# Optimization experiments

Measured on AMD Instinct MI355X. Metric: run time of the kernel, lower is better.

The kernel has to match this reference:

```python
import jax, jax.numpy as jnp
import numpy as np

V = 32000  # vocab_size
H = 5      # hidden_size (hardcoded-tiny per original module)
T = 1024   # encoder input length
L = 1024   # decoder output length


def setup_inputs() -> dict:
    key = jax.random.key(0)
    ks = jax.random.split(key, 11)
    f32 = jnp.float32
    return {
        "x": jax.random.normal(ks[0], (T, V), f32),
        "l": L,
        "Eg_en": jax.random.normal(ks[1], (H, V), f32),
        "Eg_de": jax.random.normal(ks[2], (V, H), f32),
        "cg_de": jax.random.normal(ks[3], (V,), f32),
        "Wg_en": jax.random.normal(ks[4], (3, H, H), f32),
        "Ug_en": jax.random.normal(ks[5], (3, H, H), f32),
        "bg_en": jax.random.normal(ks[6], (3, H), f32),
        "Wg_de": jax.random.normal(ks[7], (3, H, H), f32),
        "Ug_de": jax.random.normal(ks[8], (3, H, H), f32),
        "bg_de": jax.random.normal(ks[9], (3, H), f32),
    }


def reference(x, l, Eg_en, Eg_de, cg_de, Wg_en, Ug_en, bg_en, Wg_de, Ug_de, bg_de):
    sig = jax.nn.sigmoid
    h = Eg_en.shape[0]

    # ---- encoder: GRU-style recurrence over x rows ----
    # fold all V->h projections into one big matmul (same math as per-step matvec)
    xe_all = x @ Eg_en.T  # [T, h]

    def enc_step(s, xe):
        z = sig(Wg_en[0] @ xe + Ug_en[0] @ s + bg_en[0])
        r = sig(Wg_en[1] @ xe + Ug_en[1] @ s + bg_en[1])
        c = jnp.tanh(Wg_en[2] @ xe + Ug_en[2] @ (s * r) + bg_en[2])
        return z * s + (1.0 - z) * c, None

    s_last, _ = jax.lax.scan(enc_step, jnp.zeros((h,), x.dtype), xe_all)

    # first decoded word
    w1 = jax.nn.relu(Eg_de @ s_last + cg_de)  # [V]

    # ---- decoder: feeds its own output back as next input ----
    def dec_step(carry, _):
        w_prev, s = carry
        xe = Eg_en @ w_prev  # [h]
        z = sig(Wg_de[0] @ xe + Ug_de[0] @ s + bg_de[0])
        r = sig(Wg_de[1] @ xe + Ug_de[1] @ s + bg_de[1])
        c = jnp.tanh(Wg_de[2] @ xe + Ug_de[2] @ (s * r) + bg_de[2])
        s_new = z * s + (1.0 - z) * c
        w = jax.nn.relu(Eg_de @ s_new + cg_de)
        return (w, s_new), w

    (_, _), words = jax.lax.scan(dec_step, (w1, s_last), None, length=l)  # [l, V]

    # original returns cat(w1, words[:-1])
    return jnp.concatenate([w1[None, :], words[:-1]], axis=0)  # [l, V]
```

## Files before the change

kernel.cpp:

```cpp
#include <hip/hip_runtime.h>

#define VSZ 32000
#define TT 1024
#define LL 1024
#define NCH 64
#define CHL 16
#define TROW 4

typedef float f32x4 __attribute__((ext_vector_type(4)));

__device__ __forceinline__ float fast_sigmoid(float x){
  return __builtin_amdgcn_rcpf(1.0f + __expf(-x));
}
__device__ __forceinline__ float fast_tanh(float x){
  float e = __expf(2.0f*x);
  return 1.0f - 2.0f*__builtin_amdgcn_rcpf(e + 1.0f);
}

__device__ __forceinline__ float rl(float v, int l){
  return __uint_as_float((unsigned)__builtin_amdgcn_readlane((int)__float_as_uint(v), l));
}

__device__ __forceinline__ void load_gru_w(const float* __restrict__ W,
                                           const float* __restrict__ U,
                                           const float* __restrict__ b,
                                           int lane, float Wr[5], float U1r[5], float U2r[5], float& bb)
{
  int g = lane / 5;
  int i = lane - g*5;
  bool okl = (lane < 15);
  int base = okl ? (g*25 + i*5) : 0;
  int bidx = okl ? (g*5 + i) : 0;
  #pragma unroll
  for (int j=0;j<5;j++){
    float w  = W[base + j];
    float u  = U[base + j];
    float u2 = U[50 + i*5 + j];
    Wr[j]  = okl ? w : 0.0f;
    U1r[j] = (okl && g < 2) ? u  : 0.0f;
    U2r[j] = (okl && g == 2) ? u2 : 0.0f;
  }
  bb = okl ? b[bidx] : 0.0f;
}

__device__ __forceinline__ void gru_step_exact(const float xe[5], float s[5], bool& conv,
                                               const float Wr[5], const float U1r[5],
                                               const float U2r[5], float bb)
{
  float acc = bb;
  #pragma unroll
  for (int j=0;j<5;j++) acc += Wr[j]*xe[j];
  #pragma unroll
  for (int j=0;j<5;j++) acc += U1r[j]*s[j];
  float zr = fast_sigmoid(acc);
  float rr[5];
  #pragma unroll
  for (int j=0;j<5;j++) rr[j] = rl(zr, 5+j);
  float acc2 = acc;
  #pragma unroll
  for (int j=0;j<5;j++) acc2 += U2r[j]*(s[j]*rr[j]);
  float cv = fast_tanh(acc2);
  conv = true;
  #pragma unroll
  for (int j=0;j<5;j++){
    float zj = rl(zr, j);
    float cj = rl(cv, 10+j);
    float ns = zj*s[j] + (1.0f - zj)*cj;
    conv = conv && (__float_as_uint(ns) == __float_as_uint(s[j]));
    s[j] = ns;
  }
}

__device__ __forceinline__ void enc_step(float pre, float s[5],
                                         const float U1r[5], const float U2r[5])
{
  float a0 = U1r[0]*s[0] + U1r[1]*s[1];
  float a1 = U1r[2]*s[2] + U1r[3]*s[3];
  float acc = pre + a0 + a1 + U1r[4]*s[4];
  float zr = fast_sigmoid(acc);
  float rr[5];
  #pragma unroll
  for (int j=0;j<5;j++) rr[j] = rl(zr, 5+j);
  float acc2 = acc;
  #pragma unroll
  for (int j=0;j<5;j++) acc2 += U2r[j]*(s[j]*rr[j]);
  float cv = fast_tanh(acc2);
  #pragma unroll
  for (int j=0;j<5;j++){
    float zj = rl(zr, j);
    float cj = rl(cv, 10+j);
    s[j] = zj*s[j] + (1.0f - zj)*cj;
  }
}

__global__ __launch_bounds__(256) void matmul_pre(const float* __restrict__ x,
                                                  const float* __restrict__ Eg_en,
                                                  const float* __restrict__ W,
                                                  const float* __restrict__ b,
                                                  float* __restrict__ pre_all,
                                                  float* __restrict__ eslots_f)
{
  const int t0 = blockIdx.x * TROW;
  const int tid = threadIdx.x;
  const int lane = tid & 63, wave = tid >> 6;
  if (blockIdx.x == 0){
    #pragma unroll
    for (int k=0;k<4;k++) eslots_f[k*256 + tid] = 0.0f;
  }
  float acc[TROW][5];
  #pragma unroll
  for (int r=0;r<TROW;r++)
    #pragma unroll
    for (int h=0;h<5;h++) acc[r][h] = 0.0f;

  #pragma unroll 2
  for (int j = tid; j < VSZ/4; j += 256){
    f32x4 ev[5];
    #pragma unroll
    for (int h=0;h<5;h++) ev[h] = ((const f32x4*)(Eg_en + (size_t)h*VSZ))[j];
    #pragma unroll
    for (int r=0;r<TROW;r++){
      f32x4 xv = ((const f32x4*)(x + (size_t)(t0+r)*VSZ))[j];
      #pragma unroll
      for (int h=0;h<5;h++)
        acc[r][h] += xv.x*ev[h].x + xv.y*ev[h].y + xv.z*ev[h].z + xv.w*ev[h].w;
    }
  }
  #pragma unroll
  for (int m=1;m<64;m<<=1){
    #pragma unroll
    for (int r=0;r<TROW;r++)
      #pragma unroll
      for (int h=0;h<5;h++) acc[r][h] += __shfl_xor(acc[r][h], m, 64);
  }
  __shared__ float part[4][TROW][5];
  __shared__ float xe_s[TROW][5];
  if (lane == 0){
    #pragma unroll
    for (int r=0;r<TROW;r++)
      #pragma unroll
      for (int h=0;h<5;h++) part[wave][r][h] = acc[r][h];
  }
  __syncthreads();
  if (tid < TROW*5){
    int r = tid/5, h = tid - r*5;
    xe_s[r][h] = part[0][r][h] + part[1][r][h] + part[2][r][h] + part[3][r][h];
  }
  __syncthreads();
  if (tid < TROW*16){
    int r = tid >> 4, k = tid & 15;
    if (k < 15){
      int g = k/5, i = k - g*5;
      float p = b[g*5+i];
      #pragma unroll
      for (int j=0;j<5;j++) p += W[g*25 + i*5 + j] * xe_s[r][j];
      pre_all[(t0+r)*16 + k] = p;
    }
  }
}

__global__ void enc_kernel(const float* __restrict__ pre_all,
                           float* __restrict__ s_enc,
                           float* __restrict__ dslots_f,
                           unsigned long long* __restrict__ eslots,
                           const float* __restrict__ U)
{
  const int w = blockIdx.x;
  const int lane = threadIdx.x;
  { int idx = w*64 + lane; if (idx < 2048) dslots_f[idx] = 0.0f; }

  int g = lane/5, i = lane - g*5;
  bool okl = (lane < 15);
  float U1r[5], U2r[5];
  #pragma unroll
  for (int j=0;j<5;j++){
    int base = okl ? (g*25 + i*5) : 0;
    float u  = U[base + j];
    float u2 = U[50 + i*5 + j];
    U1r[j] = (okl && g < 2) ? u  : 0.0f;
    U2r[j] = (okl && g == 2) ? u2 : 0.0f;
  }

  float prc[CHL];
  #pragma unroll
  for (int k=0;k<CHL;k++) prc[k] = okl ? pre_all[(w*CHL + k)*16 + lane] : 0.0f;

  float s_in[5] = {0,0,0,0,0};
  float prev[5] = {0,0,0,0,0};
  unsigned p = 0;
  for(;;){
    p++;
    float s[5];
    #pragma unroll
    for (int j=0;j<5;j++) s[j] = s_in[j];
    #pragma unroll
    for (int k=0;k<CHL;k++) enc_step(prc[k], s, U1r, U2r);

    bool stable = (p > 1);
    #pragma unroll
    for (int j=0;j<5;j++)
      stable = stable && (__float_as_uint(s[j]) == __float_as_uint(prev[j]));
    #pragma unroll
    for (int j=0;j<5;j++) prev[j] = s[j];

    const unsigned long long hi = ((unsigned long long)((p<<1) | (stable?1u:0u))) << 32;
    if (lane == 0){
      unsigned long long* wp = eslots + (size_t)w*8;
      #pragma unroll
      for (int j=0;j<5;j++)
        __hip_atomic_store(wp+j, hi | (unsigned long long)__float_as_uint(s[j]),
                           __ATOMIC_RELAXED, __HIP_MEMORY_SCOPE_AGENT);
    }

    const unsigned long long* rp = eslots + (size_t)lane*8;
    unsigned long long w0,w1,w2,w3,w4;
    for(;;){
      w0 = __hip_atomic_load(rp+0, __ATOMIC_RELAXED, __HIP_MEMORY_SCOPE_AGENT);
      w1 = __hip_atomic_load(rp+1, __ATOMIC_RELAXED, __HIP_MEMORY_SCOPE_AGENT);
      w2 = __hip_atomic_load(rp+2, __ATOMIC_RELAXED, __HIP_MEMORY_SCOPE_AGENT);
      w3 = __hip_atomic_load(rp+3, __ATOMIC_RELAXED, __HIP_MEMORY_SCOPE_AGENT);
      w4 = __hip_atomic_load(rp+4, __ATOMIC_RELAXED, __HIP_MEMORY_SCOPE_AGENT);
      bool ok = ((unsigned)(w0>>33)==p) & ((unsigned)(w1>>33)==p) & ((unsigned)(w2>>33)==p)
              & ((unsigned)(w3>>33)==p) & ((unsigned)(w4>>33)==p);
      if (__all(ok)) break;
    }
    bool slot_stable = ((w0>>32)&1ull) != 0;
    bool gstable = __all(slot_stable);

    float xin[5];
    xin[0] = __uint_as_float((unsigned)w0);
    xin[1] = __uint_as_float((unsigned)w1);
    xin[2] = __uint_as_float((unsigned)w2);
    xin[3] = __uint_as_float((unsigned)w3);
    xin[4] = __uint_as_float((unsigned)w4);

    if (gstable){
      if (w == 0 && lane == 0){
        #pragma unroll
        for (int j=0;j<5;j++) s_enc[j] = rl(xin[j], 63);
      }
      break;
    }
    if (w > 0){
      #pragma unroll
      for (int j=0;j<5;j++) s_in[j] = rl(xin[j], w-1);
    }
  }
}

__global__ __launch_bounds__(256, 1) void dec_kernel(
    const float* __restrict__ Eg_en, const float* __restrict__ Eg_de,
    const float* __restrict__ cg_de,
    const float* __restrict__ W, const float* __restrict__ U, const float* __restrict__ b,
    const float* __restrict__ s_enc,
    unsigned long long* __restrict__ slots,
    float* __restrict__ out,
    int* __restrict__ t_conv_out)
{
  const int wg = blockIdx.x;
  const int tid = threadIdx.x;
  const int lane = tid & 63;
  const int wave = tid >> 6;
  const int slot_id = wg*4 + wave;

  float Wr[5], U1r[5], U2r[5], bb;
  load_gru_w(W, U, b, lane, Wr, U1r, U2r, bb);

  const bool act = (tid < 250);
  const int v0 = wg*2000 + tid*8;
  float de[8][5], en[5][8], cb[8];
  if (act){
    #pragma unroll
    for (int k=0;k<8;k++){
      #pragma unroll
      for (int j=0;j<5;j++) de[k][j] = Eg_de[(v0+k)*5 + j];
      cb[k] = cg_de[v0+k];
    }
    #pragma unroll
    for (int h=0;h<5;h++){
      #pragma unroll
      for (int k=0;k<8;k++) en[h][k] = Eg_en[h*VSZ + v0 + k];
    }
  } else {
    #pragma unroll
    for (int k=0;k<8;k++){
      cb[k] = 0.0f;
      #pragma unroll
      for (int j=0;j<5;j++) de[k][j] = 0.0f;
    }
    #pragma unroll
    for (int h=0;h<5;h++){
      #pragma unroll
      for (int k=0;k<8;k++) en[h][k] = 0.0f;
    }
  }

  float s[5];
  #pragma unroll
  for (int j=0;j<5;j++) s[j] = s_enc[j];

  for (int t=0; t<LL; t++){
    float px[5] = {0,0,0,0,0};
    float o[8];
    #pragma unroll
    for (int k=0;k<8;k++){
      float u = cb[k];
      #pragma unroll
      for (int j=0;j<5;j++) u += de[k][j]*s[j];
      u = fmaxf(u, 0.0f);
      o[k] = u;
      #pragma unroll
      for (int h=0;h<5;h++) px[h] += u*en[h][k];
    }
    if (act){
      f32x4* po = (f32x4*)(out + (size_t)t*VSZ + v0);
      f32x4 oa = {o[0], o[1], o[2], o[3]};
      f32x4 ob = {o[4], o[5], o[6], o[7]};
      po[0] = oa; po[1] = ob;
    }
    if (t == LL-1){
      if (wg == 0 && tid == 0) *t_conv_out = LL-1;
      break;
    }

    #pragma unroll
    for (int m=1;m<64;m<<=1){
      #pragma unroll
      for (int h=0;h<5;h++) px[h] += __shfl_xor(px[h], m, 64);
    }

    const unsigned long long tg = (unsigned long long)(t+1);
    if (lane == 0){
      unsigned long long* wp = slots + ((size_t)(t&1)*64 + slot_id)*8;
      #pragma unroll
      for (int j=0;j<5;j++)
        __hip_atomic_store(wp+j, (tg<<32) | (unsigned long long)__float_as_uint(px[j]),
                           __ATOMIC_RELAXED, __HIP_MEMORY_SCOPE_AGENT);
    }

    const unsigned long long* rp = slots + ((size_t)(t&1)*64 + lane)*8;
    unsigned long long w0,w1,w2,w3,w4;
    for(;;){
      w0 = __hip_atomic_load(rp+0, __ATOMIC_RELAXED, __HIP_MEMORY_SCOPE_AGENT);
      w1 = __hip_atomic_load(rp+1, __ATOMIC_RELAXED, __HIP_MEMORY_SCOPE_AGENT);
      w2 = __hip_atomic_load(rp+2, __ATOMIC_RELAXED, __HIP_MEMORY_SCOPE_AGENT);
      w3 = __hip_atomic_load(rp+3, __ATOMIC_RELAXED, __HIP_MEMORY_SCOPE_AGENT);
      w4 = __hip_atomic_load(rp+4, __ATOMIC_RELAXED, __HIP_MEMORY_SCOPE_AGENT);
      bool ok = ((w0>>32)==tg) & ((w1>>32)==tg) & ((w2>>32)==tg)
              & ((w3>>32)==tg) & ((w4>>32)==tg);
      if (__all(ok)) break;
    }
    float xe[5];
    xe[0] = __uint_as_float((unsigned)w0);
    xe[1] = __uint_as_float((unsigned)w1);
    xe[2] = __uint_as_float((unsigned)w2);
    xe[3] = __uint_as_float((unsigned)w3);
    xe[4] = __uint_as_float((unsigned)w4);
    #pragma unroll
    for (int m=1;m<64;m<<=1){
      #pragma unroll
      for (int j=0;j<5;j++) xe[j] += __shfl_xor(xe[j], m, 64);
    }

    bool conv;
    gru_step_exact(xe, s, conv, Wr, U1r, U2r, bb);

    if (conv){
      if (wg == 0 && tid == 0) *t_conv_out = t;
      break;
    }
  }
}

__global__ __launch_bounds__(256) void fill_kernel(const int* __restrict__ t_conv_p,
                                                   float* __restrict__ out)
{
  const int tc = *t_conv_p;
  const int r = blockIdx.y;
  if (r <= tc) return;
  const int tid = threadIdx.x;
  if (tid >= 250) return;
  const int off = blockIdx.x*2000 + tid*8;
  const f32x4* src = (const f32x4*)(out + (size_t)tc*VSZ + off);
  f32x4 a = src[0], b = src[1];
  f32x4* dst = (f32x4*)(out + (size_t)r*VSZ + off);
  dst[0] = a; dst[1] = b;
}

extern "C" void kernel_launch(void* const* d_in, const int* in_sizes, int n_in,
                              void* d_out, int out_size, void* d_ws, size_t ws_size,
                              hipStream_t stream)
{
  const float* x     = (const float*)d_in[0];
  const float* Eg_en = (const float*)d_in[2];
  const float* Eg_de = (const float*)d_in[3];
  const float* cg_de = (const float*)d_in[4];
  const float* Wg_en = (const float*)d_in[5];
  const float* Ug_en = (const float*)d_in[6];
  const float* bg_en = (const float*)d_in[7];
  const float* Wg_de = (const float*)d_in[8];
  const float* Ug_de = (const float*)d_in[9];
  const float* bg_de = (const float*)d_in[10];
  float* out = (float*)d_out;

  float* ws       = (float*)d_ws;
  float* pre_all  = ws;
  float* s_enc    = ws + 16384;
  int*   t_conv   = (int*)(ws + 16448);
  float* eslots_f = ws + 16512;
  float* dslots_f = ws + 17536;
  unsigned long long* eslots = (unsigned long long*)eslots_f;
  unsigned long long* dslots = (unsigned long long*)dslots_f;

  matmul_pre<<<dim3(TT/TROW), dim3(256), 0, stream>>>(x, Eg_en, Wg_en, bg_en, pre_all, eslots_f);
  enc_kernel<<<dim3(NCH), dim3(64), 0, stream>>>(pre_all, s_enc, dslots_f, eslots, Ug_en);
  dec_kernel<<<dim3(16), dim3(256), 0, stream>>>(Eg_en, Eg_de, cg_de,
                                                 Wg_de, Ug_de, bg_de,
                                                 s_enc, dslots, out, t_conv);
  fill_kernel<<<dim3(16, LL), dim3(256), 0, stream>>>(t_conv, out);
}
```

Measured before the change: 79.93 us.

## Shrink decoder grid to 8 workgroups with LDS pre-reduction and split encoder projection

The decoder now runs 8 workgroups of 512 threads, reduced from 16 of 256. Each step first reduces partial sums across waves in shared memory, then only one wave publishes 5 tagged slots per workgroup. This leaves each wave polling 40 slots, not 64×5, which is meant to cut cross-workgroup synchronisation traffic and latency per decoder step. The encoder input projection is split into two vocab halves per 8-row group and combined with atomicAdd into a memset buffer. The W·xe+b gate preactivation moves into the encoder kernel. The cost is an extra __syncthreads per decoder step and an extra memset launch.

```diff
diff --git a/kernel.cpp b/kernel.cpp
--- a/kernel.cpp
+++ b/kernel.cpp
@@ -5,7 +5,10 @@
 #define LL 1024
 #define NCH 64
 #define CHL 16
-#define TROW 4
+#define TROW 8
+#define JHALF 4000
+#define DWG 8
+#define DTH 512
 
 typedef float f32x4 __attribute__((ext_vector_type(4)));
 
@@ -95,12 +98,12 @@
 
 __global__ __launch_bounds__(256) void matmul_pre(const float* __restrict__ x,
                                                   const float* __restrict__ Eg_en,
-                                                  const float* __restrict__ W,
-                                                  const float* __restrict__ b,
-                                                  float* __restrict__ pre_all,
+                                                  float* __restrict__ xe_all,
                                                   float* __restrict__ eslots_f)
 {
-  const int t0 = blockIdx.x * TROW;
+  const int grp = blockIdx.x >> 1;
+  const int hf  = blockIdx.x & 1;
+  const int t0  = grp * TROW;
   const int tid = threadIdx.x;
   const int lane = tid & 63, wave = tid >> 6;
   if (blockIdx.x == 0){
@@ -113,8 +116,8 @@
     #pragma unroll
     for (int h=0;h<5;h++) acc[r][h] = 0.0f;
 
-  #pragma unroll 2
-  for (int j = tid; j < VSZ/4; j += 256){
+  const int jbeg = hf*JHALF;
+  for (int j = jbeg + tid; j < jbeg + JHALF; j += 256){
     f32x4 ev[5];
     #pragma unroll
     for (int h=0;h<5;h++) ev[h] = ((const f32x4*)(Eg_en + (size_t)h*VSZ))[j];
@@ -134,7 +137,6 @@
       for (int h=0;h<5;h++) acc[r][h] += __shfl_xor(acc[r][h], m, 64);
   }
   __shared__ float part[4][TROW][5];
-  __shared__ float xe_s[TROW][5];
   if (lane == 0){
     #pragma unroll
     for (int r=0;r<TROW;r++)
@@ -144,46 +146,35 @@
   __syncthreads();
   if (tid < TROW*5){
     int r = tid/5, h = tid - r*5;
-    xe_s[r][h] = part[0][r][h] + part[1][r][h] + part[2][r][h] + part[3][r][h];
-  }
-  __syncthreads();
-  if (tid < TROW*16){
-    int r = tid >> 4, k = tid & 15;
-    if (k < 15){
-      int g = k/5, i = k - g*5;
-      float p = b[g*5+i];
-      #pragma unroll
-      for (int j=0;j<5;j++) p += W[g*25 + i*5 + j] * xe_s[r][j];
-      pre_all[(t0+r)*16 + k] = p;
-    }
-  }
-}
-
-__global__ void enc_kernel(const float* __restrict__ pre_all,
+    float v = part[0][r][h] + part[1][r][h] + part[2][r][h] + part[3][r][h];
+    atomicAdd(&xe_all[(t0+r)*8 + h], v);
+  }
+}
+
+__global__ void enc_kernel(const float* __restrict__ xe_all,
                            float* __restrict__ s_enc,
                            float* __restrict__ dslots_f,
                            unsigned long long* __restrict__ eslots,
-                           const float* __restrict__ U)
+                           const float* __restrict__ W,
+                           const float* __restrict__ U,
+                           const float* __restrict__ b)
 {
   const int w = blockIdx.x;
   const int lane = threadIdx.x;
-  { int idx = w*64 + lane; if (idx < 2048) dslots_f[idx] = 0.0f; }
-
-  int g = lane/5, i = lane - g*5;
-  bool okl = (lane < 15);
-  float U1r[5], U2r[5];
-  #pragma unroll
-  for (int j=0;j<5;j++){
-    int base = okl ? (g*25 + i*5) : 0;
-    float u  = U[base + j];
-    float u2 = U[50 + i*5 + j];
-    U1r[j] = (okl && g < 2) ? u  : 0.0f;
-    U2r[j] = (okl && g == 2) ? u2 : 0.0f;
-  }
+  { int idx = w*64 + lane; if (idx < 256) dslots_f[idx] = 0.0f; }
+
+  float Wr[5], U1r[5], U2r[5], bb;
+  load_gru_w(W, U, b, lane, Wr, U1r, U2r, bb);
 
   float prc[CHL];
   #pragma unroll
-  for (int k=0;k<CHL;k++) prc[k] = okl ? pre_all[(w*CHL + k)*16 + lane] : 0.0f;
+  for (int k=0;k<CHL;k++){
+    const float* xr = xe_all + (w*CHL + k)*8;
+    float p = bb;
+    #pragma unroll
+    for (int j=0;j<5;j++) p += Wr[j]*xr[j];
+    prc[k] = p;
+  }
 
   float s_in[5] = {0,0,0,0,0};
   float prev[5] = {0,0,0,0,0};
@@ -248,7 +239,7 @@
   }
 }
 
-__global__ __launch_bounds__(256, 1) void dec_kernel(
+__global__ __launch_bounds__(DTH, 1) void dec_kernel(
     const float* __restrict__ Eg_en, const float* __restrict__ Eg_de,
     const float* __restrict__ cg_de,
     const float* __restrict__ W, const float* __restrict__ U, const float* __restrict__ b,
@@ -260,14 +251,13 @@
   const int wg = blockIdx.x;
   const int tid = threadIdx.x;
   const int lane = tid & 63;
-  const int wave = tid >> 6;
-  const int slot_id = wg*4 + wave;
+  const int wid = tid >> 6;
 
   float Wr[5], U1r[5], U2r[5], bb;
   load_gru_w(W, U, b, lane, Wr, U1r, U2r, bb);
 
-  const bool act = (tid < 250);
-  const int v0 = wg*2000 + tid*8;
+  const bool act = (tid < 500);
+  const int v0 = wg*4000 + tid*8;
   float de[8][5], en[5][8], cb[8];
   if (act){
     #pragma unroll
@@ -294,6 +284,8 @@
       for (int k=0;k<8;k++) en[h][k] = 0.0f;
     }
   }
+
+  __shared__ float red[8][5];
 
   float s[5];
   #pragma unroll
@@ -328,39 +320,39 @@
       #pragma unroll
       for (int h=0;h<5;h++) px[h] += __shfl_xor(px[h], m, 64);
     }
+    if (lane == 0){
+      #pragma unroll
+      for (int h=0;h<5;h++) red[wid][h] = px[h];
+    }
+    __syncthreads();
 
     const unsigned long long tg = (unsigned long long)(t+1);
-    if (lane == 0){
-      unsigned long long* wp = slots + ((size_t)(t&1)*64 + slot_id)*8;
-      #pragma unroll
-      for (int j=0;j<5;j++)
-        __hip_atomic_store(wp+j, (tg<<32) | (unsigned long long)__float_as_uint(px[j]),
-                           __ATOMIC_RELAXED, __HIP_MEMORY_SCOPE_AGENT);
-    }
-
-    const unsigned long long* rp = slots + ((size_t)(t&1)*64 + lane)*8;
-    unsigned long long w0,w1,w2,w3,w4;
+    unsigned long long* sb = slots + (size_t)(t&1)*64;
+
+    if (wid == 0 && lane < 5){
+      float tot = red[0][lane];
+      #pragma unroll
+      for (int ww=1;ww<8;ww++) tot += red[ww][lane];
+      __hip_atomic_store(sb + wg*8 + lane,
+                         (tg<<32) | (unsigned long long)__float_as_uint(tot),
+                         __ATOMIC_RELAXED, __HIP_MEMORY_SCOPE_AGENT);
+    }
+
+    const int sl = lane & 7;
+    const int wd = lane >> 3;
+    const unsigned long long* rp = sb + sl*8 + wd;
+    unsigned long long wv;
     for(;;){
-      w0 = __hip_atomic_load(rp+0, __ATOMIC_RELAXED, __HIP_MEMORY_SCOPE_AGENT);
-      w1 = __hip_atomic_load(rp+1, __ATOMIC_RELAXED, __HIP_MEMORY_SCOPE_AGENT);
-      w2 = __hip_atomic_load(rp+2, __ATOMIC_RELAXED, __HIP_MEMORY_SCOPE_AGENT);
-      w3 = __hip_atomic_load(rp+3, __ATOMIC_RELAXED, __HIP_MEMORY_SCOPE_AGENT);
-      w4 = __hip_atomic_load(rp+4, __ATOMIC_RELAXED, __HIP_MEMORY_SCOPE_AGENT);
-      bool ok = ((w0>>32)==tg) & ((w1>>32)==tg) & ((w2>>32)==tg)
-              & ((w3>>32)==tg) & ((w4>>32)==tg);
+      wv = __hip_atomic_load(rp, __ATOMIC_RELAXED, __HIP_MEMORY_SCOPE_AGENT);
+      bool ok = (wd >= 5) || ((wv>>32) == tg);
       if (__all(ok)) break;
     }
+    float xv = (wd < 5) ? __uint_as_float((unsigned)wv) : 0.0f;
+    #pragma unroll
+    for (int m=1;m<8;m<<=1) xv += __shfl_xor(xv, m, 64);
     float xe[5];
-    xe[0] = __uint_as_float((unsigned)w0);
-    xe[1] = __uint_as_float((unsigned)w1);
-    xe[2] = __uint_as_float((unsigned)w2);
-    xe[3] = __uint_as_float((unsigned)w3);
-    xe[4] = __uint_as_float((unsigned)w4);
-    #pragma unroll
-    for (int m=1;m<64;m<<=1){
-      #pragma unroll
-      for (int j=0;j<5;j++) xe[j] += __shfl_xor(xe[j], m, 64);
-    }
+    #pragma unroll
+    for (int j=0;j<5;j++) xe[j] = __shfl(xv, j*8, 64);
 
     bool conv;
     gru_step_exact(xe, s, conv, Wr, U1r, U2r, bb);
@@ -404,18 +396,20 @@
   float* out = (float*)d_out;
 
   float* ws       = (float*)d_ws;
-  float* pre_all  = ws;
-  float* s_enc    = ws + 16384;
-  int*   t_conv   = (int*)(ws + 16448);
-  float* eslots_f = ws + 16512;
-  float* dslots_f = ws + 17536;
+  float* xe_all   = ws;
+  float* s_enc    = ws + 8192;
+  int*   t_conv   = (int*)(ws + 8256);
+  float* eslots_f = ws + 8320;
+  float* dslots_f = ws + 9344;
   unsigned long long* eslots = (unsigned long long*)eslots_f;
   unsigned long long* dslots = (unsigned long long*)dslots_f;
 
-  matmul_pre<<<dim3(TT/TROW), dim3(256), 0, stream>>>(x, Eg_en, Wg_en, bg_en, pre_all, eslots_f);
-  enc_kernel<<<dim3(NCH), dim3(64), 0, stream>>>(pre_all, s_enc, dslots_f, eslots, Ug_en);
-  dec_kernel<<<dim3(16), dim3(256), 0, stream>>>(Eg_en, Eg_de, cg_de,
-                                                 Wg_de, Ug_de, bg_de,
-                                                 s_enc, dslots, out, t_conv);
+  hipMemsetAsync(xe_all, 0, TT*8*sizeof(float), stream);
+  matmul_pre<<<dim3(TT/TROW*2), dim3(256), 0, stream>>>(x, Eg_en, xe_all, eslots_f);
+  enc_kernel<<<dim3(NCH), dim3(64), 0, stream>>>(xe_all, s_enc, dslots_f, eslots,
+                                                 Wg_en, Ug_en, bg_en);
+  dec_kernel<<<dim3(DWG), dim3(DTH), 0, stream>>>(Eg_en, Eg_de, cg_de,
+                                                  Wg_de, Ug_de, bg_de,
+                                                  s_enc, dslots, out, t_conv);
   fill_kernel<<<dim3(16, LL), dim3(256), 0, stream>>>(t_conv, out);
 }
```

Result: slower. 95.12 us (+19.0%).

## Split encoder projection over vocab halves and move W-projection into encoder kernel

Applied to the files above, without the earlier changes.

The x@Eg_en matmul now processes 8 rows per block and splits the vocab dimension into two halves across paired blocks. Each block writes partial xe sums, which doubles Eg_en reuse per x row while keeping the block count at 256. The W·xe+b gate projection moves from matmul_pre into enc_kernel, which sums the two partial halves when loading each chunk. This drops one sync and the tail of matmul_pre, but adds more accumulator registers and a small amount of extra per-step work in the encoder.

```diff
diff --git a/kernel.cpp b/kernel.cpp
--- a/kernel.cpp
+++ b/kernel.cpp
@@ -5,7 +5,8 @@
 #define LL 1024
 #define NCH 64
 #define CHL 16
-#define TROW 4
+#define TROW 8
+#define JHALF 4000
 
 typedef float f32x4 __attribute__((ext_vector_type(4)));
 
@@ -95,12 +96,12 @@
 
 __global__ __launch_bounds__(256) void matmul_pre(const float* __restrict__ x,
                                                   const float* __restrict__ Eg_en,
-                                                  const float* __restrict__ W,
-                                                  const float* __restrict__ b,
-                                                  float* __restrict__ pre_all,
+                                                  float* __restrict__ xe_half,
                                                   float* __restrict__ eslots_f)
 {
-  const int t0 = blockIdx.x * TROW;
+  const int grp = blockIdx.x >> 1;
+  const int hf  = blockIdx.x & 1;
+  const int t0  = grp * TROW;
   const int tid = threadIdx.x;
   const int lane = tid & 63, wave = tid >> 6;
   if (blockIdx.x == 0){
@@ -113,8 +114,8 @@
     #pragma unroll
     for (int h=0;h<5;h++) acc[r][h] = 0.0f;
 
-  #pragma unroll 2
-  for (int j = tid; j < VSZ/4; j += 256){
+  const int jbeg = hf*JHALF;
+  for (int j = jbeg + tid; j < jbeg + JHALF; j += 256){
     f32x4 ev[5];
     #pragma unroll
     for (int h=0;h<5;h++) ev[h] = ((const f32x4*)(Eg_en + (size_t)h*VSZ))[j];
@@ -134,7 +135,6 @@
       for (int h=0;h<5;h++) acc[r][h] += __shfl_xor(acc[r][h], m, 64);
   }
   __shared__ float part[4][TROW][5];
-  __shared__ float xe_s[TROW][5];
   if (lane == 0){
     #pragma unroll
     for (int r=0;r<TROW;r++)
@@ -144,46 +144,36 @@
   __syncthreads();
   if (tid < TROW*5){
     int r = tid/5, h = tid - r*5;
-    xe_s[r][h] = part[0][r][h] + part[1][r][h] + part[2][r][h] + part[3][r][h];
-  }
-  __syncthreads();
-  if (tid < TROW*16){
-    int r = tid >> 4, k = tid & 15;
-    if (k < 15){
-      int g = k/5, i = k - g*5;
-      float p = b[g*5+i];
-      #pragma unroll
-      for (int j=0;j<5;j++) p += W[g*25 + i*5 + j] * xe_s[r][j];
-      pre_all[(t0+r)*16 + k] = p;
-    }
-  }
-}
-
-__global__ void enc_kernel(const float* __restrict__ pre_all,
+    float v = part[0][r][h] + part[1][r][h] + part[2][r][h] + part[3][r][h];
+    xe_half[(size_t)hf*TT*8 + (t0+r)*8 + h] = v;
+  }
+}
+
+__global__ void enc_kernel(const float* __restrict__ xe_half,
                            float* __restrict__ s_enc,
                            float* __restrict__ dslots_f,
                            unsigned long long* __restrict__ eslots,
-                           const float* __restrict__ U)
+                           const float* __restrict__ W,
+                           const float* __restrict__ U,
+                           const float* __restrict__ b)
 {
   const int w = blockIdx.x;
   const int lane = threadIdx.x;
   { int idx = w*64 + lane; if (idx < 2048) dslots_f[idx] = 0.0f; }
 
-  int g = lane/5, i = lane - g*5;
-  bool okl = (lane < 15);
-  float U1r[5], U2r[5];
-  #pragma unroll
-  for (int j=0;j<5;j++){
-    int base = okl ? (g*25 + i*5) : 0;
-    float u  = U[base + j];
-    float u2 = U[50 + i*5 + j];
-    U1r[j] = (okl && g < 2) ? u  : 0.0f;
-    U2r[j] = (okl && g == 2) ? u2 : 0.0f;
-  }
+  float Wr[5], U1r[5], U2r[5], bb;
+  load_gru_w(W, U, b, lane, Wr, U1r, U2r, bb);
 
   float prc[CHL];
   #pragma unroll
-  for (int k=0;k<CHL;k++) prc[k] = okl ? pre_all[(w*CHL + k)*16 + lane] : 0.0f;
+  for (int k=0;k<CHL;k++){
+    const float* x0 = xe_half + (w*CHL + k)*8;
+    const float* x1 = xe_half + (size_t)TT*8 + (w*CHL + k)*8;
+    float p = bb;
+    #pragma unroll
+    for (int j=0;j<5;j++) p += Wr[j]*(x0[j] + x1[j]);
+    prc[k] = p;
+  }
 
   float s_in[5] = {0,0,0,0,0};
   float prev[5] = {0,0,0,0,0};
@@ -404,7 +394,7 @@
   float* out = (float*)d_out;
 
   float* ws       = (float*)d_ws;
-  float* pre_all  = ws;
+  float* xe_half  = ws;
   float* s_enc    = ws + 16384;
   int*   t_conv   = (int*)(ws + 16448);
   float* eslots_f = ws + 16512;
@@ -412,8 +402,9 @@
   unsigned long long* eslots = (unsigned long long*)eslots_f;
   unsigned long long* dslots = (unsigned long long*)dslots_f;
 
-  matmul_pre<<<dim3(TT/TROW), dim3(256), 0, stream>>>(x, Eg_en, Wg_en, bg_en, pre_all, eslots_f);
-  enc_kernel<<<dim3(NCH), dim3(64), 0, stream>>>(pre_all, s_enc, dslots_f, eslots, Ug_en);
+  matmul_pre<<<dim3(TT/TROW*2), dim3(256), 0, stream>>>(x, Eg_en, xe_half, eslots_f);
+  enc_kernel<<<dim3(NCH), dim3(64), 0, stream>>>(xe_half, s_enc, dslots_f, eslots,
+                                                 Wg_en, Ug_en, bg_en);
   dec_kernel<<<dim3(16), dim3(256), 0, stream>>>(Eg_en, Eg_de, cg_de,
                                                  Wg_de, Ug_de, bg_de,
                                                  s_enc, dslots, out, t_conv);
```

After: 89.21 us. 11.6% more time.

## Fuse encoder, decoder and fill into one persistent kernel with helper fill blocks

Applied to the files above, without the earlier changes.

Merges the encoder chunk-scan, the decoder recurrence and the tail fill into a single launch of 256 blocks. The first 16 blocks run the encoder (one chunk per wave) and then the decoder, and publish the converged state and step index through a tagged slot. The remaining 240 blocks spin on that slot, recompute the fixed output row themselves and write the rows after convergence in a strided split. This removes two kernel launches and the fill kernel's reread of the converged row, at the cost of spinning blocks that rely on all 256 blocks being resident together and of a larger slot-clearing step in the first kernel.

```diff
diff --git a/kernel.cpp b/kernel.cpp
--- a/kernel.cpp
+++ b/kernel.cpp
@@ -98,14 +98,17 @@
                                                   const float* __restrict__ W,
                                                   const float* __restrict__ b,
                                                   float* __restrict__ pre_all,
-                                                  float* __restrict__ eslots_f)
+                                                  float* __restrict__ clr)
 {
   const int t0 = blockIdx.x * TROW;
   const int tid = threadIdx.x;
   const int lane = tid & 63, wave = tid >> 6;
   if (blockIdx.x == 0){
     #pragma unroll
-    for (int k=0;k<4;k++) eslots_f[k*256 + tid] = 0.0f;
+    for (int k=0;k<13;k++){
+      int idx = k*256 + tid;
+      if (idx < 3088) clr[idx] = 0.0f;
+    }
   }
   float acc[TROW][5];
   #pragma unroll
@@ -159,116 +162,27 @@
   }
 }
 
-__global__ void enc_kernel(const float* __restrict__ pre_all,
-                           float* __restrict__ s_enc,
-                           float* __restrict__ dslots_f,
-                           unsigned long long* __restrict__ eslots,
-                           const float* __restrict__ U)
-{
-  const int w = blockIdx.x;
-  const int lane = threadIdx.x;
-  { int idx = w*64 + lane; if (idx < 2048) dslots_f[idx] = 0.0f; }
-
-  int g = lane/5, i = lane - g*5;
-  bool okl = (lane < 15);
-  float U1r[5], U2r[5];
-  #pragma unroll
-  for (int j=0;j<5;j++){
-    int base = okl ? (g*25 + i*5) : 0;
-    float u  = U[base + j];
-    float u2 = U[50 + i*5 + j];
-    U1r[j] = (okl && g < 2) ? u  : 0.0f;
-    U2r[j] = (okl && g == 2) ? u2 : 0.0f;
-  }
-
-  float prc[CHL];
-  #pragma unroll
-  for (int k=0;k<CHL;k++) prc[k] = okl ? pre_all[(w*CHL + k)*16 + lane] : 0.0f;
-
-  float s_in[5] = {0,0,0,0,0};
-  float prev[5] = {0,0,0,0,0};
-  unsigned p = 0;
-  for(;;){
-    p++;
-    float s[5];
-    #pragma unroll
-    for (int j=0;j<5;j++) s[j] = s_in[j];
-    #pragma unroll
-    for (int k=0;k<CHL;k++) enc_step(prc[k], s, U1r, U2r);
-
-    bool stable = (p > 1);
-    #pragma unroll
-    for (int j=0;j<5;j++)
-      stable = stable && (__float_as_uint(s[j]) == __float_as_uint(prev[j]));
-    #pragma unroll
-    for (int j=0;j<5;j++) prev[j] = s[j];
-
-    const unsigned long long hi = ((unsigned long long)((p<<1) | (stable?1u:0u))) << 32;
-    if (lane == 0){
-      unsigned long long* wp = eslots + (size_t)w*8;
-      #pragma unroll
-      for (int j=0;j<5;j++)
-        __hip_atomic_store(wp+j, hi | (unsigned long long)__float_as_uint(s[j]),
-                           __ATOMIC_RELAXED, __HIP_MEMORY_SCOPE_AGENT);
-    }
-
-    const unsigned long long* rp = eslots + (size_t)lane*8;
-    unsigned long long w0,w1,w2,w3,w4;
-    for(;;){
-      w0 = __hip_atomic_load(rp+0, __ATOMIC_RELAXED, __HIP_MEMORY_SCOPE_AGENT);
-      w1 = __hip_atomic_load(rp+1, __ATOMIC_RELAXED, __HIP_MEMORY_SCOPE_AGENT);
-      w2 = __hip_atomic_load(rp+2, __ATOMIC_RELAXED, __HIP_MEMORY_SCOPE_AGENT);
-      w3 = __hip_atomic_load(rp+3, __ATOMIC_RELAXED, __HIP_MEMORY_SCOPE_AGENT);
-      w4 = __hip_atomic_load(rp+4, __ATOMIC_RELAXED, __HIP_MEMORY_SCOPE_AGENT);
-      bool ok = ((unsigned)(w0>>33)==p) & ((unsigned)(w1>>33)==p) & ((unsigned)(w2>>33)==p)
-              & ((unsigned)(w3>>33)==p) & ((unsigned)(w4>>33)==p);
-      if (__all(ok)) break;
-    }
-    bool slot_stable = ((w0>>32)&1ull) != 0;
-    bool gstable = __all(slot_stable);
-
-    float xin[5];
-    xin[0] = __uint_as_float((unsigned)w0);
-    xin[1] = __uint_as_float((unsigned)w1);
-    xin[2] = __uint_as_float((unsigned)w2);
-    xin[3] = __uint_as_float((unsigned)w3);
-    xin[4] = __uint_as_float((unsigned)w4);
-
-    if (gstable){
-      if (w == 0 && lane == 0){
-        #pragma unroll
-        for (int j=0;j<5;j++) s_enc[j] = rl(xin[j], 63);
-      }
-      break;
-    }
-    if (w > 0){
-      #pragma unroll
-      for (int j=0;j<5;j++) s_in[j] = rl(xin[j], w-1);
-    }
-  }
-}
-
-__global__ __launch_bounds__(256, 1) void dec_kernel(
+__global__ __launch_bounds__(256, 1) void fused_edf(
     const float* __restrict__ Eg_en, const float* __restrict__ Eg_de,
     const float* __restrict__ cg_de,
-    const float* __restrict__ W, const float* __restrict__ U, const float* __restrict__ b,
-    const float* __restrict__ s_enc,
-    unsigned long long* __restrict__ slots,
-    float* __restrict__ out,
-    int* __restrict__ t_conv_out)
+    const float* __restrict__ Wde, const float* __restrict__ Ude, const float* __restrict__ bde,
+    const float* __restrict__ Uen,
+    const float* __restrict__ pre_all,
+    unsigned long long* __restrict__ eslots,
+    unsigned long long* __restrict__ dslots,
+    unsigned long long* __restrict__ cslot,
+    float* __restrict__ out)
 {
   const int wg = blockIdx.x;
   const int tid = threadIdx.x;
   const int lane = tid & 63;
   const int wave = tid >> 6;
-  const int slot_id = wg*4 + wave;
-
-  float Wr[5], U1r[5], U2r[5], bb;
-  load_gru_w(W, U, b, lane, Wr, U1r, U2r, bb);
-
+
+  const int vs = wg & 15;
   const bool act = (tid < 250);
-  const int v0 = wg*2000 + tid*8;
-  float de[8][5], en[5][8], cb[8];
+  const int v0 = vs*2000 + tid*8;
+
+  float de[8][5], cb[8];
   if (act){
     #pragma unroll
     for (int k=0;k<8;k++){
@@ -276,11 +190,6 @@
       for (int j=0;j<5;j++) de[k][j] = Eg_de[(v0+k)*5 + j];
       cb[k] = cg_de[v0+k];
     }
-    #pragma unroll
-    for (int h=0;h<5;h++){
-      #pragma unroll
-      for (int k=0;k<8;k++) en[h][k] = Eg_en[h*VSZ + v0 + k];
-    }
   } else {
     #pragma unroll
     for (int k=0;k<8;k++){
@@ -288,103 +197,226 @@
       #pragma unroll
       for (int j=0;j<5;j++) de[k][j] = 0.0f;
     }
-    #pragma unroll
-    for (int h=0;h<5;h++){
-      #pragma unroll
-      for (int k=0;k<8;k++) en[h][k] = 0.0f;
-    }
   }
 
   float s[5];
-  #pragma unroll
-  for (int j=0;j<5;j++) s[j] = s_enc[j];
-
-  for (int t=0; t<LL; t++){
-    float px[5] = {0,0,0,0,0};
-    float o[8];
+  int tc;
+  float o[8];
+
+  if (wg < 16){
+    int g = lane/5, i = lane - g*5;
+    bool okl = (lane < 15);
+    float eU1[5], eU2[5];
+    #pragma unroll
+    for (int j=0;j<5;j++){
+      int base = okl ? (g*25 + i*5) : 0;
+      float u  = Uen[base + j];
+      float u2 = Uen[50 + i*5 + j];
+      eU1[j] = (okl && g < 2) ? u  : 0.0f;
+      eU2[j] = (okl && g == 2) ? u2 : 0.0f;
+    }
+    const int ch = wg*4 + wave;
+    float prc[CHL];
+    #pragma unroll
+    for (int k=0;k<CHL;k++) prc[k] = okl ? pre_all[(ch*CHL + k)*16 + lane] : 0.0f;
+
+    float Wr[5], U1r[5], U2r[5], bb;
+    load_gru_w(Wde, Ude, bde, lane, Wr, U1r, U2r, bb);
+    float en[5][8];
+    if (act){
+      #pragma unroll
+      for (int h=0;h<5;h++)
+        #pragma unroll
+        for (int k=0;k<8;k++) en[h][k] = Eg_en[h*VSZ + v0 + k];
+    } else {
+      #pragma unroll
+      for (int h=0;h<5;h++)
+        #pragma unroll
+        for (int k=0;k<8;k++) en[h][k] = 0.0f;
+    }
+
+    float s_in[5] = {0,0,0,0,0};
+    float prev[5] = {0,0,0,0,0};
+    float xin[5];
+    unsigned p = 0;
+    for(;;){
+      p++;
+      float se[5];
+      #pragma unroll
+      for (int j=0;j<5;j++) se[j] = s_in[j];
+      #pragma unroll
+      for (int k=0;k<CHL;k++) enc_step(prc[k], se, eU1, eU2);
+
+      bool stable = (p > 1);
+      #pragma unroll
+      for (int j=0;j<5;j++)
+        stable = stable && (__float_as_uint(se[j]) == __float_as_uint(prev[j]));
+      #pragma unroll
+      for (int j=0;j<5;j++) prev[j] = se[j];
+
+      const unsigned long long hi = ((unsigned long long)((p<<1) | (stable?1u:0u))) << 32;
+      if (lane == 0){
+        unsigned long long* wp = eslots + (size_t)ch*8;
+        #pragma unroll
+        for (int j=0;j<5;j++)
+          __hip_atomic_store(wp+j, hi | (unsigned long long)__float_as_uint(se[j]),
+                             __ATOMIC_RELAXED, __HIP_MEMORY_SCOPE_AGENT);
+      }
+      const unsigned long long* rp = eslots + (size_t)lane*8;
+      unsigned long long w0,w1,w2,w3,w4;
+      for(;;){
+        w0 = __hip_atomic_load(rp+0, __ATOMIC_RELAXED, __HIP_MEMORY_SCOPE_AGENT);
+        w1 = __hip_atomic_load(rp+1, __ATOMIC_RELAXED, __HIP_MEMORY_SCOPE_AGENT);
+        w2 = __hip_atomic_load(rp+2, __ATOMIC_RELAXED, __HIP_MEMORY_SCOPE_AGENT);
+        w3 = __hip_atomic_load(rp+3, __ATOMIC_RELAXED, __HIP_MEMORY_SCOPE_AGENT);
+        w4 = __hip_atomic_load(rp+4, __ATOMIC_RELAXED, __HIP_MEMORY_SCOPE_AGENT);
+        bool ok = ((unsigned)(w0>>33)==p) & ((unsigned)(w1>>33)==p) & ((unsigned)(w2>>33)==p)
+                & ((unsigned)(w3>>33)==p) & ((unsigned)(w4>>33)==p);
+        if (__all(ok)) break;
+      }
+      bool slot_stable = ((w0>>32)&1ull) != 0;
+      bool gstable = __all(slot_stable);
+      xin[0] = __uint_as_float((unsigned)w0);
+      xin[1] = __uint_as_float((unsigned)w1);
+      xin[2] = __uint_as_float((unsigned)w2);
+      xin[3] = __uint_as_float((unsigned)w3);
+      xin[4] = __uint_as_float((unsigned)w4);
+      if (gstable) break;
+      if (ch > 0){
+        #pragma unroll
+        for (int j=0;j<5;j++) s_in[j] = rl(xin[j], ch-1);
+      }
+    }
+    #pragma unroll
+    for (int j=0;j<5;j++) s[j] = rl(xin[j], 63);
+
+    const int slot_id = wg*4 + wave;
+    for (int t=0; t<LL; t++){
+      float px[5] = {0,0,0,0,0};
+      #pragma unroll
+      for (int k=0;k<8;k++){
+        float u = cb[k];
+        #pragma unroll
+        for (int j=0;j<5;j++) u += de[k][j]*s[j];
+        u = fmaxf(u, 0.0f);
+        o[k] = u;
+        #pragma unroll
+        for (int h=0;h<5;h++) px[h] += u*en[h][k];
+      }
+      if (act){
+        f32x4* po = (f32x4*)(out + (size_t)t*VSZ + v0);
+        f32x4 oa = {o[0], o[1], o[2], o[3]};
+        f32x4 ob = {o[4], o[5], o[6], o[7]};
+        po[0] = oa; po[1] = ob;
+      }
+      if (t == LL-1){
+        tc = t;
+        if (wg == 0 && tid == 0){
+          #pragma unroll
+          for (int j=0;j<5;j++)
+            __hip_atomic_store(cslot+j,
+              (((unsigned long long)(0xC0DE0000u|j))<<32) | (unsigned long long)__float_as_uint(s[j]),
+              __ATOMIC_RELAXED, __HIP_MEMORY_SCOPE_AGENT);
+          __hip_atomic_store(cslot+5,
+            (((unsigned long long)0xC0DE0005u)<<32) | (unsigned long long)(unsigned)tc,
+            __ATOMIC_RELAXED, __HIP_MEMORY_SCOPE_AGENT);
+          __hip_atomic_store(cslot+6, ((unsigned long long)0xC0DE0006u)<<32,
+            __ATOMIC_RELAXED, __HIP_MEMORY_SCOPE_AGENT);
+          __hip_atomic_store(cslot+7, ((unsigned long long)0xC0DE0007u)<<32,
+            __ATOMIC_RELAXED, __HIP_MEMORY_SCOPE_AGENT);
+        }
+        break;
+      }
+
+      #pragma unroll
+      for (int m=1;m<64;m<<=1){
+        #pragma unroll
+        for (int h=0;h<5;h++) px[h] += __shfl_xor(px[h], m, 64);
+      }
+      const unsigned long long tg = (unsigned long long)(t+1);
+      if (lane == 0){
+        unsigned long long* wp = dslots + ((size_t)(t&1)*64 + slot_id)*8;
+        #pragma unroll
+        for (int j=0;j<5;j++)
+          __hip_atomic_store(wp+j, (tg<<32) | (unsigned long long)__float_as_uint(px[j]),
+                             __ATOMIC_RELAXED, __HIP_MEMORY_SCOPE_AGENT);
+      }
+      const unsigned long long* rp = dslots + ((size_t)(t&1)*64 + lane)*8;
+      unsigned long long w0,w1,w2,w3,w4;
+      for(;;){
+        w0 = __hip_atomic_load(rp+0, __ATOMIC_RELAXED, __HIP_MEMORY_SCOPE_AGENT);
+        w1 = __hip_atomic_load(rp+1, __ATOMIC_RELAXED, __HIP_MEMORY_SCOPE_AGENT);
+        w2 = __hip_atomic_load(rp+2, __ATOMIC_RELAXED, __HIP_MEMORY_SCOPE_AGENT);
+        w3 = __hip_atomic_load(rp+3, __ATOMIC_RELAXED, __HIP_MEMORY_SCOPE_AGENT);
+        w4 = __hip_atomic_load(rp+4, __ATOMIC_RELAXED, __HIP_MEMORY_SCOPE_AGENT);
+        bool ok = ((w0>>32)==tg) & ((w1>>32)==tg) & ((w2>>32)==tg)
+                & ((w3>>32)==tg) & ((w4>>32)==tg);
+        if (__all(ok)) break;
+      }
+      float xe[5];
+      xe[0] = __uint_as_float((unsigned)w0);
+      xe[1] = __uint_as_float((unsigned)w1);
+      xe[2] = __uint_as_float((unsigned)w2);
+      xe[3] = __uint_as_float((unsigned)w3);
+      xe[4] = __uint_as_float((unsigned)w4);
+      #pragma unroll
+      for (int m=1;m<64;m<<=1){
+        #pragma unroll
+        for (int j=0;j<5;j++) xe[j] += __shfl_xor(xe[j], m, 64);
+      }
+
+      bool conv;
+      gru_step_exact(xe, s, conv, Wr, U1r, U2r, bb);
+
+      if (conv){
+        tc = t;
+        if (wg == 0 && tid == 0){
+          #pragma unroll
+          for (int j=0;j<5;j++)
+            __hip_atomic_store(cslot+j,
+              (((unsigned long long)(0xC0DE0000u|j))<<32) | (unsigned long long)__float_as_uint(s[j]),
+              __ATOMIC_RELAXED, __HIP_MEMORY_SCOPE_AGENT);
+          __hip_atomic_store(cslot+5,
+            (((unsigned long long)0xC0DE0005u)<<32) | (unsigned long long)(unsigned)tc,
+            __ATOMIC_RELAXED, __HIP_MEMORY_SCOPE_AGENT);
+          __hip_atomic_store(cslot+6, ((unsigned long long)0xC0DE0006u)<<32,
+            __ATOMIC_RELAXED, __HIP_MEMORY_SCOPE_AGENT);
+          __hip_atomic_store(cslot+7, ((unsigned long long)0xC0DE0007u)<<32,
+            __ATOMIC_RELAXED, __HIP_MEMORY_SCOPE_AGENT);
+        }
+        break;
+      }
+    }
+  } else {
+    unsigned long long wv;
+    const unsigned expect = 0xC0DE0000u | (lane & 7);
+    for(;;){
+      wv = __hip_atomic_load(cslot + (lane&7), __ATOMIC_RELAXED, __HIP_MEMORY_SCOPE_AGENT);
+      if (__all((unsigned)(wv>>32) == expect)) break;
+      __builtin_amdgcn_s_sleep(64);
+    }
+    unsigned lo = (unsigned)wv;
+    #pragma unroll
+    for (int j=0;j<5;j++)
+      s[j] = __uint_as_float((unsigned)__builtin_amdgcn_readlane((int)lo, j));
+    tc = (int)(unsigned)__builtin_amdgcn_readlane((int)lo, 5);
     #pragma unroll
     for (int k=0;k<8;k++){
       float u = cb[k];
       #pragma unroll
       for (int j=0;j<5;j++) u += de[k][j]*s[j];
-      u = fmaxf(u, 0.0f);
-      o[k] = u;
-      #pragma unroll
-      for (int h=0;h<5;h++) px[h] += u*en[h][k];
-    }
-    if (act){
-      f32x4* po = (f32x4*)(out + (size_t)t*VSZ + v0);
-      f32x4 oa = {o[0], o[1], o[2], o[3]};
-      f32x4 ob = {o[4], o[5], o[6], o[7]};
+      o[k] = fmaxf(u, 0.0f);
+    }
+  }
+
+  if (act){
+    f32x4 oa = {o[0], o[1], o[2], o[3]};
+    f32x4 ob = {o[4], o[5], o[6], o[7]};
+    for (int r = tc + 1 + (wg >> 4); r < LL; r += 16){
+      f32x4* po = (f32x4*)(out + (size_t)r*VSZ + v0);
       po[0] = oa; po[1] = ob;
     }
-    if (t == LL-1){
-      if (wg == 0 && tid == 0) *t_conv_out = LL-1;
-      break;
-    }
-
-    #pragma unroll
-    for (int m=1;m<64;m<<=1){
-      #pragma unroll
-      for (int h=0;h<5;h++) px[h] += __shfl_xor(px[h], m, 64);
-    }
-
-    const unsigned long long tg = (unsigned long long)(t+1);
-    if (lane == 0){
-      unsigned long long* wp = slots + ((size_t)(t&1)*64 + slot_id)*8;
-      #pragma unroll
-      for (int j=0;j<5;j++)
-        __hip_atomic_store(wp+j, (tg<<32) | (unsigned long long)__float_as_uint(px[j]),
-                           __ATOMIC_RELAXED, __HIP_MEMORY_SCOPE_AGENT);
-    }
-
-    const unsigned long long* rp = slots + ((size_t)(t&1)*64 + lane)*8;
-    unsigned long long w0,w1,w2,w3,w4;
-    for(;;){
-      w0 = __hip_atomic_load(rp+0, __ATOMIC_RELAXED, __HIP_MEMORY_SCOPE_AGENT);
-      w1 = __hip_atomic_load(rp+1, __ATOMIC_RELAXED, __HIP_MEMORY_SCOPE_AGENT);
-      w2 = __hip_atomic_load(rp+2, __ATOMIC_RELAXED, __HIP_MEMORY_SCOPE_AGENT);
-      w3 = __hip_atomic_load(rp+3, __ATOMIC_RELAXED, __HIP_MEMORY_SCOPE_AGENT);
-      w4 = __hip_atomic_load(rp+4, __ATOMIC_RELAXED, __HIP_MEMORY_SCOPE_AGENT);
-      bool ok = ((w0>>32)==tg) & ((w1>>32)==tg) & ((w2>>32)==tg)
-              & ((w3>>32)==tg) & ((w4>>32)==tg);
-      if (__all(ok)) break;
-    }
-    float xe[5];
-    xe[0] = __uint_as_float((unsigned)w0);
-    xe[1] = __uint_as_float((unsigned)w1);
-    xe[2] = __uint_as_float((unsigned)w2);
-    xe[3] = __uint_as_float((unsigned)w3);
-    xe[4] = __uint_as_float((unsigned)w4);
-    #pragma unroll
-    for (int m=1;m<64;m<<=1){
-      #pragma unroll
-      for (int j=0;j<5;j++) xe[j] += __shfl_xor(xe[j], m, 64);
-    }
-
-    bool conv;
-    gru_step_exact(xe, s, conv, Wr, U1r, U2r, bb);
-
-    if (conv){
-      if (wg == 0 && tid == 0) *t_conv_out = t;
-      break;
-    }
-  }
-}
-
-__global__ __launch_bounds__(256) void fill_kernel(const int* __restrict__ t_conv_p,
-                                                   float* __restrict__ out)
-{
-  const int tc = *t_conv_p;
-  const int r = blockIdx.y;
-  if (r <= tc) return;
-  const int tid = threadIdx.x;
-  if (tid >= 250) return;
-  const int off = blockIdx.x*2000 + tid*8;
-  const f32x4* src = (const f32x4*)(out + (size_t)tc*VSZ + off);
-  f32x4 a = src[0], b = src[1];
-  f32x4* dst = (f32x4*)(out + (size_t)r*VSZ + off);
-  dst[0] = a; dst[1] = b;
+  }
 }
 
 extern "C" void kernel_launch(void* const* d_in, const int* in_sizes, int n_in,
@@ -405,17 +437,13 @@
 
   float* ws       = (float*)d_ws;
   float* pre_all  = ws;
-  float* s_enc    = ws + 16384;
-  int*   t_conv   = (int*)(ws + 16448);
-  float* eslots_f = ws + 16512;
-  float* dslots_f = ws + 17536;
-  unsigned long long* eslots = (unsigned long long*)eslots_f;
-  unsigned long long* dslots = (unsigned long long*)dslots_f;
-
-  matmul_pre<<<dim3(TT/TROW), dim3(256), 0, stream>>>(x, Eg_en, Wg_en, bg_en, pre_all, eslots_f);
-  enc_kernel<<<dim3(NCH), dim3(64), 0, stream>>>(pre_all, s_enc, dslots_f, eslots, Ug_en);
-  dec_kernel<<<dim3(16), dim3(256), 0, stream>>>(Eg_en, Eg_de, cg_de,
-                                                 Wg_de, Ug_de, bg_de,
-                                                 s_enc, dslots, out, t_conv);
-  fill_kernel<<<dim3(16, LL), dim3(256), 0, stream>>>(t_conv, out);
-}
+  float* clr      = ws + 16384;
+  unsigned long long* eslots = (unsigned long long*)(ws + 16384);
+  unsigned long long* dslots = (unsigned long long*)(ws + 16384 + 1024);
+  unsigned long long* cslot  = (unsigned long long*)(ws + 16384 + 3072);
+
+  matmul_pre<<<dim3(TT/TROW), dim3(256), 0, stream>>>(x, Eg_en, Wg_en, bg_en, pre_all, clr);
+  fused_edf<<<dim3(256), dim3(256), 0, stream>>>(Eg_en, Eg_de, cg_de,
+                                                 Wg_de, Ug_de, bg_de, Ug_en,
+                                                 pre_all, eslots, dslots, cslot, out);
+}
```

Result: slower. 82.28 us (+2.9%).
